# Kernel tuning notes

Hardware: AMD Instinct MI355X
Metric: run time of the kernel (lower is better)

## Reference

```python
import jax, jax.numpy as jnp
import numpy as np

B_GRAPHS = 32
EMB = 512
ESM = 1280
HEADS = 8
HEAD_DIM = EMB // HEADS


def _segments():
    lengths = 256 + 8 * np.arange(B_GRAPHS)          # 256..504, N = 12160
    batch_ids = np.repeat(np.arange(B_GRAPHS), lengths).astype(np.int32)
    pos = np.concatenate([np.arange(l) for l in lengths]).astype(np.int32)
    return batch_ids, pos, int(lengths.max()), int(lengths.sum())


def setup_inputs() -> dict:
    key = jax.random.key(0)
    ks = jax.random.split(key, 10)
    batch_ids, pos, pad_len, n = _segments()
    s = 0.02
    return {
        "esm_embedding": jax.random.normal(ks[0], (n, ESM), jnp.float32),
        "h": jax.random.normal(ks[1], (n, EMB), jnp.float32),
        "W_esm": jax.random.normal(ks[2], (EMB, ESM), jnp.float32) * s,
        "b_esm": jnp.zeros((EMB,), jnp.float32),
        "Wq": jax.random.normal(ks[3], (EMB, EMB), jnp.float32) * s,
        "bq": jnp.zeros((EMB,), jnp.float32),
        "Wk": jax.random.normal(ks[4], (EMB, EMB), jnp.float32) * s,
        "bk": jnp.zeros((EMB,), jnp.float32),
        "Wv": jax.random.normal(ks[5], (EMB, EMB), jnp.float32) * s,
        "bv": jnp.zeros((EMB,), jnp.float32),
        "Wo": jax.random.normal(ks[6], (EMB, EMB), jnp.float32) * s,
        "bo": jnp.zeros((EMB,), jnp.float32),
        "gamma": jnp.ones((EMB,), jnp.float32),
        "beta": jnp.zeros((EMB,), jnp.float32),
        "batch_ids": jnp.asarray(batch_ids),
        "pos": jnp.asarray(pos),
        "pad_len": pad_len,
        "num_graphs": B_GRAPHS,
    }


def _layer_norm(x, gamma, beta, eps=1e-5):
    mu = jnp.mean(x, axis=-1, keepdims=True)
    var = jnp.var(x, axis=-1, keepdims=True)
    return (x - mu) * jax.lax.rsqrt(var + eps) * gamma + beta


def reference(esm_embedding, h, W_esm, b_esm, Wq, bq, Wk, bk, Wv, bv, Wo, bo,
              gamma, beta, batch_ids, pos, pad_len, num_graphs):
    B, P, D, H, hd = num_graphs, pad_len, EMB, HEADS, HEAD_DIM
    residual = h
    # to_dense_batch: scatter nodes into [B, P, *] padded tensors + key mask
    h_dense = jnp.zeros((B, P, D), h.dtype).at[batch_ids, pos].set(h)
    h_mask = jnp.zeros((B, P), bool).at[batch_ids, pos].set(True)
    h_esm = esm_embedding @ W_esm.T + b_esm                      # [N, D]
    esm_dense = jnp.zeros((B, P, D), h.dtype).at[batch_ids, pos].set(h_esm)

    q = (h_dense @ Wq.T + bq).reshape(B, P, H, hd)
    k = (esm_dense @ Wk.T + bk).reshape(B, P, H, hd)
    v = (esm_dense @ Wv.T + bv).reshape(B, P, H, hd)

    scores = jnp.einsum("bqhd,bkhd->bhqk", q, k) / jnp.sqrt(jnp.float32(hd))
    scores = jnp.where(h_mask[:, None, None, :], scores, -jnp.inf)
    attn = jax.nn.softmax(scores, axis=-1)                        # [B,H,P,P]
    out = jnp.einsum("bhqk,bkhd->bqhd", attn, v).reshape(B, P, D)
    out = out @ Wo.T + bo
    out = out[batch_ids, pos]                                     # unpad -> [N, D]
    return _layer_norm(out + residual, gamma, beta)
```

## Files before the change

### kernel.cpp

```cpp
#include <hip/hip_runtime.h>

#define NTOT 12160
#define EMBD 512
#define ESMD 1280
#define NHEAD 8
#define HD 64
#define NG 32
#define NTILE 768

typedef __attribute__((ext_vector_type(8))) short short8v;
typedef __attribute__((ext_vector_type(4))) short short4v;
typedef __attribute__((ext_vector_type(4))) float floatx4;

__device__ inline short f2bf(float f) {
  union { float f; unsigned u; } v; v.f = f;
  unsigned r = v.u + 0x7fffu + ((v.u >> 16) & 1u);
  return (short)(r >> 16);
}

__device__ inline void gload_lds16(const void* g, void* l) {
  __builtin_amdgcn_global_load_lds((const __attribute__((address_space(1))) void*)g,
                                   (__attribute__((address_space(3))) void*)l, 16, 0, 0);
}

__device__ inline int node_graph(int n) {
  int g = (int)((sqrtf(3969.f + (float)n) - 63.f) * 0.5f);
  if (4 * (g + 1) * (g + 64) <= n) g++;
  else if (4 * g * (g + 63) > n) g--;
  return g;
}

__global__ __launch_bounds__(256) void cvt_kernel(
    const float* __restrict__ esm, const float* __restrict__ h,
    const float* __restrict__ Wq, const float* __restrict__ Wk,
    const float* __restrict__ Wv, const float* __restrict__ Wo,
    short* __restrict__ esm_b, short* __restrict__ h_b, short* __restrict__ Wq_b,
    short* __restrict__ Wk_b, short* __restrict__ Wv_b, short* __restrict__ Wo_b)
{
  int idx = blockIdx.x * 256 + threadIdx.x;
  const float* src; short* dst; int off;
  if      (idx < 3891200) { src = esm; dst = esm_b; off = idx; }
  else if (idx < 5447680) { src = h;   dst = h_b;   off = idx - 3891200; }
  else if (idx < 5513216) { src = Wq;  dst = Wq_b;  off = idx - 5447680; }
  else if (idx < 5578752) { src = Wk;  dst = Wk_b;  off = idx - 5513216; }
  else if (idx < 5644288) { src = Wv;  dst = Wv_b;  off = idx - 5578752; }
  else                    { src = Wo;  dst = Wo_b;  off = idx - 5644288; }
  const float4 v = *(const float4*)&src[(size_t)off * 4];
  short4v s; s[0] = f2bf(v.x); s[1] = f2bf(v.y); s[2] = f2bf(v.z); s[3] = f2bf(v.w);
  *(short4v*)&dst[(size_t)off * 4] = s;
}

__global__ __launch_bounds__(256) void wtrans_kernel(
    const float* __restrict__ W, short* __restrict__ WT)
{
  __shared__ short t[32][33];
  const int c0 = blockIdx.x * 32;
  const int r0 = blockIdx.y * 32;
  const int tr = threadIdx.x >> 5, tc = threadIdx.x & 31;
  for (int i = 0; i < 4; i++)
    t[i * 8 + tr][tc] = f2bf(W[(size_t)(r0 + i * 8 + tr) * 1280 + c0 + tc]);
  __syncthreads();
  for (int i = 0; i < 4; i++)
    WT[(size_t)(c0 + i * 8 + tr) * 512 + r0 + tc] = t[tc][i * 8 + tr];
}

__global__ __launch_bounds__(256) void bfuse_kernel(
    const float* __restrict__ Wk, const float* __restrict__ Wv,
    const float* __restrict__ besm, const float* __restrict__ bk,
    const float* __restrict__ bv, float* __restrict__ bkp, float* __restrict__ bvp)
{
  int wgid = blockIdx.x * 4 + (threadIdx.x >> 6);
  int lane = threadIdx.x & 63;
  const float* W  = (wgid < 512) ? Wk : Wv;
  const float* ba = (wgid < 512) ? bk : bv;
  float* o        = (wgid < 512) ? bkp : bvp;
  int row = wgid & 511;
  const float4 w0 = *(const float4*)&W[(size_t)row * 512 + lane * 8];
  const float4 w1 = *(const float4*)&W[(size_t)row * 512 + lane * 8 + 4];
  const float4 b0 = *(const float4*)&besm[lane * 8];
  const float4 b1 = *(const float4*)&besm[lane * 8 + 4];
  float s = w0.x * b0.x + w0.y * b0.y + w0.z * b0.z + w0.w * b0.w
          + w1.x * b1.x + w1.y * b1.y + w1.z * b1.z + w1.w * b1.w;
  for (int off = 1; off < 64; off <<= 1) s += __shfl_xor(s, off);
  if (lane == 0) o[row] = s + ba[row];
}

__device__ inline void gemm_core(const short* __restrict__ A, const short* __restrict__ W,
                                 int K, int row0, int col0,
                                 short* As, short* Bs, floatx4 acc[4][4])
{
  const int tid = threadIdx.x;
  const int lane = tid & 63, wave = tid >> 6;
  const int l15 = lane & 15, quad = lane >> 4;
  const int wm = (wave >> 1) * 64, wn = (wave & 1) * 64;
  const int lrow = lane >> 3;
  const int scol = ((lane & 7) ^ lrow) * 8;
  const int swz = l15 & 7;

  for (int k0 = 0; k0 < K; k0 += 64) {
    if (k0) __syncthreads();
    for (int p = 0; p < 4; p++) {
      int seg = wave * 4 + p;
      gload_lds16(&A[(size_t)(row0 + seg * 8 + lrow) * K + k0 + scol], &As[seg * 512]);
    }
    for (int p = 0; p < 4; p++) {
      int seg = wave * 4 + p;
      gload_lds16(&W[(size_t)(col0 + seg * 8 + lrow) * K + k0 + scol], &Bs[seg * 512]);
    }
    __syncthreads();
    for (int ks = 0; ks < 64; ks += 32) {
      const int off = (((ks >> 3) + quad) ^ swz) << 3;
      short8v a[4], b[4];
      for (int mt = 0; mt < 4; mt++)
        a[mt] = *(const short8v*)&As[(wm + mt * 16 + l15) * 64 + off];
      for (int nt = 0; nt < 4; nt++)
        b[nt] = *(const short8v*)&Bs[(wn + nt * 16 + l15) * 64 + off];
      for (int mt = 0; mt < 4; mt++)
        for (int nt = 0; nt < 4; nt++)
          acc[mt][nt] = __builtin_amdgcn_mfma_f32_16x16x32_bf16(a[mt], b[nt], acc[mt][nt], 0, 0, 0);
    }
  }
}

__device__ inline void epi_bf16(floatx4 acc[4][4], const float* bias, short* C,
                                int row0, int col0, int wm, int wn, int l15, int quad)
{
  for (int nt = 0; nt < 4; nt++) {
    int col = col0 + wn + nt * 16 + l15;
    float bv = bias[col];
    for (int mt = 0; mt < 4; mt++) {
      int rowb = row0 + wm + mt * 16 + quad * 4;
      for (int r = 0; r < 4; r++)
        C[(size_t)(rowb + r) * EMBD + col] = f2bf(acc[mt][nt][r] + bv);
    }
  }
}

__global__ __launch_bounds__(256) void wfuse_gemm(
    const short* __restrict__ Wk_b, const short* __restrict__ Wv_b,
    const short* __restrict__ WT, short* __restrict__ Wkp, short* __restrict__ Wvp)
{
  __shared__ short As[128 * 64];
  __shared__ short Bs[128 * 64];
  const int wh = blockIdx.x >= 10;
  const int col0 = (blockIdx.x - (wh ? 10 : 0)) * 128;
  const int row0 = blockIdx.y * 128;
  floatx4 acc[4][4];
  for (int i = 0; i < 4; i++) for (int j = 0; j < 4; j++)
    for (int r = 0; r < 4; r++) acc[i][j][r] = 0.f;
  gemm_core(wh ? Wv_b : Wk_b, WT, 512, row0, col0, As, Bs, acc);
  short* O = wh ? Wvp : Wkp;
  const int lane = threadIdx.x & 63, wave = threadIdx.x >> 6;
  const int l15 = lane & 15, quad = lane >> 4;
  const int wm = (wave >> 1) * 64, wn = (wave & 1) * 64;
  for (int nt = 0; nt < 4; nt++) {
    int col = col0 + wn + nt * 16 + l15;
    for (int mt = 0; mt < 4; mt++) {
      int rowb = row0 + wm + mt * 16 + quad * 4;
      for (int r = 0; r < 4; r++)
        O[(size_t)(rowb + r) * ESMD + col] = f2bf(acc[mt][nt][r]);
    }
  }
}

__global__ __launch_bounds__(512) void qkv_gemm(
    const short* __restrict__ hb, const short* __restrict__ esm_b,
    const short* __restrict__ Wq_b, const short* __restrict__ Wkp, const short* __restrict__ Wvp,
    const float* __restrict__ bq, const float* __restrict__ bkp, const float* __restrict__ bvp,
    short* __restrict__ qb, short* __restrict__ kp, short* __restrict__ vp)
{
  __shared__ short As[128 * 64];
  __shared__ short Bs[256 * 64];
  const int bid = blockIdx.x;
  const int xcd = bid & 7, idx = bid >> 3;
  const int rowc = idx / 6, c = idx - rowc * 6;
  const int r = xcd + 8 * rowc;
  if (r >= 95) return;
  const int row0 = r * 128;
  const int col0 = (c & 1) * 256;
  const int which = c >> 1;
  const short* A = (which == 0) ? hb : esm_b;
  const short* W = (which == 0) ? Wq_b : (which == 1 ? Wkp : Wvp);
  const int K = (which == 0) ? 512 : 1280;

  const int tid = threadIdx.x;
  const int lane = tid & 63, wave = tid >> 6;
  const int l15 = lane & 15, quad = lane >> 4;
  const int wm = (wave >> 2) * 64, wn = (wave & 3) * 64;
  const int lrow = lane >> 3;
  const int scol = ((lane & 7) ^ lrow) * 8;
  const int swz = l15 & 7;

  floatx4 acc[4][4];
  for (int i = 0; i < 4; i++) for (int j = 0; j < 4; j++)
    for (int rr = 0; rr < 4; rr++) acc[i][j][rr] = 0.f;

  for (int k0 = 0; k0 < K; k0 += 64) {
    if (k0) __syncthreads();
    for (int p = 0; p < 2; p++) {
      int seg = wave * 2 + p;
      gload_lds16(&A[(size_t)(row0 + seg * 8 + lrow) * K + k0 + scol], &As[seg * 512]);
    }
    for (int p = 0; p < 4; p++) {
      int seg = wave * 4 + p;
      gload_lds16(&W[(size_t)(col0 + seg * 8 + lrow) * K + k0 + scol], &Bs[seg * 512]);
    }
    __syncthreads();
    for (int ks = 0; ks < 64; ks += 32) {
      const int off = (((ks >> 3) + quad) ^ swz) << 3;
      short8v a[4], b[4];
      for (int mt = 0; mt < 4; mt++)
        a[mt] = *(const short8v*)&As[(wm + mt * 16 + l15) * 64 + off];
      for (int nt = 0; nt < 4; nt++)
        b[nt] = *(const short8v*)&Bs[(wn + nt * 16 + l15) * 64 + off];
      for (int mt = 0; mt < 4; mt++)
        for (int nt = 0; nt < 4; nt++)
          acc[mt][nt] = __builtin_amdgcn_mfma_f32_16x16x32_bf16(a[mt], b[nt], acc[mt][nt], 0, 0, 0);
    }
  }

  if (which == 0) {
    epi_bf16(acc, bq, qb, row0, col0, wm, wn, l15, quad);
  } else if (which == 1) {
    for (int mt = 0; mt < 4; mt++) {
      int rowb = row0 + wm + mt * 16 + quad * 4;
      int g = node_graph(rowb);
      int loc = rowb - 4 * g * (g + 63);
      int ptile = 16 * g + (g * g) / 4 + (loc >> 4);
      int l15k = loc & 15;
      for (int nt = 0; nt < 4; nt++) {
        int col = col0 + wn + nt * 16 + l15;
        float bv = bkp[col];
        int hh = col >> 6, dh = col & 63;
        int hfh = dh >> 5, qk = (dh & 31) >> 3, jk = dh & 7;
        size_t base = ((size_t)(hh * NTILE + ptile) * 2 + hfh) * 512
                      + (size_t)l15k * 32 + qk * 8 + jk;
        for (int rr = 0; rr < 4; rr++)
          kp[base + (size_t)rr * 32] = f2bf(acc[mt][nt][rr] + bv);
      }
    }
  } else {
    for (int mt = 0; mt < 4; mt++) {
      int rowb = row0 + wm + mt * 16 + quad * 4;
      int g = node_graph(rowb);
      int loc = rowb - 4 * g * (g + 63);
      int ptile = 16 * g + (g * g) / 4 + (loc >> 4);
      int koff = loc & 15;
      for (int nt = 0; nt < 4; nt++) {
        int col = col0 + wn + nt * 16 + l15;
        float bv = bvp[col];
        int hh = col >> 6, dh = col & 63;
        int dt = dh >> 4, l15v = dh & 15;
        size_t base = ((size_t)(hh * 4 + dt) * NTILE + ptile) * 256
                      + (size_t)l15v * 16 + koff;
        short4v sv;
        for (int rr = 0; rr < 4; rr++) sv[rr] = f2bf(acc[mt][nt][rr] + bv);
        *(short4v*)&vp[base] = sv;
      }
    }
  }
}

template<bool MASK>
__device__ inline void attn_chunk(
    int kc, int L, int Tg, int hb, int hdt4,
    const short* __restrict__ kp, const short* __restrict__ vp,
    short* Ps, const short8v& aq0, const short8v& aq1,
    floatx4 oacc[4], float rowsum[4], int l15, int quad)
{
  floatx4 s[4];
  const int t0 = Tg + (kc >> 4);
  for (int sub = 0; sub < 4; sub++) {
    const short* kpt = &kp[((size_t)(hb + t0 + sub) * 2) * 512 + l15 * 32 + quad * 8];
    short8v b0 = *(const short8v*)kpt;
    short8v b1 = *(const short8v*)(kpt + 512);
    floatx4 c; for (int r = 0; r < 4; r++) c[r] = 0.f;
    c = __builtin_amdgcn_mfma_f32_16x16x32_bf16(aq0, b0, c, 0, 0, 0);
    c = __builtin_amdgcn_mfma_f32_16x16x32_bf16(aq1, b1, c, 0, 0, 0);
    s[sub] = c;
  }
  for (int sub = 0; sub < 4; sub++)
    for (int r = 0; r < 4; r++) {
      float p = __expf(s[sub][r] * 0.125f);
      if (MASK && (kc + sub * 16 + l15 >= L)) p = 0.f;
      rowsum[r] += p;
      Ps[(quad * 4 + r) * 72 + sub * 16 + l15] = f2bf(p);
    }
  for (int half = 0; half < 2; half++) {
    short8v pA = *(const short8v*)&Ps[l15 * 72 + half * 32 + quad * 8];
    for (int dt = 0; dt < 4; dt++) {
      size_t vbase = ((size_t)(hdt4 + dt) * NTILE + t0 + half * 2 + (quad >> 1)) * 256
                     + (size_t)l15 * 16 + (quad & 1) * 8;
      short8v bvv = *(const short8v*)&vp[vbase];
      oacc[dt] = __builtin_amdgcn_mfma_f32_16x16x32_bf16(pA, bvv, oacc[dt], 0, 0, 0);
    }
  }
}

__global__ __launch_bounds__(512) void attn_kernel(
    const short* __restrict__ qb, const short* __restrict__ kp,
    const short* __restrict__ vp, short* __restrict__ ao)
{
  __shared__ short Ps_all[8][16 * 72];
  const int x = blockIdx.x & 7, j = blockIdx.x >> 3;
  int g = -1, qt = 0, accum = 0;
  for (int i = 0; i < 4; i++) {
    int gg = x + 8 * i;
    int t = 16 + ((gg + 1) >> 1);
    if (j < accum + t) { g = gg; qt = j - accum; break; }
    accum += t;
  }
  if (g < 0) return;
  const int L = 256 + 8 * g;
  const int start = 4 * g * (g + 63);
  const int Tg = 16 * g + (g * g) / 4;
  const int h = threadIdx.x >> 6;
  const int lane = threadIdx.x & 63;
  const int l15 = lane & 15, quad = lane >> 4;
  const int hb = h * NTILE, hdt4 = h * 4;
  short* Ps = Ps_all[h];

  int qrow = qt * 16 + l15;
  if (qrow > L - 1) qrow = L - 1;
  const size_t qoff = (size_t)(start + qrow) * EMBD + h * HD + quad * 8;
  const short8v aq0 = *(const short8v*)&qb[qoff];
  const short8v aq1 = *(const short8v*)&qb[qoff + 32];

  float rowsum[4];
  floatx4 oacc[4];
  for (int r = 0; r < 4; r++) rowsum[r] = 0.f;
  for (int dt = 0; dt < 4; dt++)
    for (int r = 0; r < 4; r++) oacc[dt][r] = 0.f;

  const int Lfull = L & ~63;
  for (int kc = 0; kc < Lfull; kc += 64)
    attn_chunk<false>(kc, L, Tg, hb, hdt4, kp, vp, Ps, aq0, aq1, oacc, rowsum, l15, quad);
  if (Lfull < L)
    attn_chunk<true>(Lfull, L, Tg, hb, hdt4, kp, vp, Ps, aq0, aq1, oacc, rowsum, l15, quad);

  float inv[4];
  for (int r = 0; r < 4; r++) {
    float red = rowsum[r];
    red += __shfl_xor(red, 1); red += __shfl_xor(red, 2);
    red += __shfl_xor(red, 4); red += __shfl_xor(red, 8);
    inv[r] = 1.f / red;
  }
  for (int dt = 0; dt < 4; dt++)
    for (int r = 0; r < 4; r++) {
      int rl = qt * 16 + quad * 4 + r;
      if (rl < L)
        ao[(size_t)(start + rl) * EMBD + h * HD + dt * 16 + l15] = f2bf(oacc[dt][r] * inv[r]);
    }
}

__global__ __launch_bounds__(256) void o_gemm(
    const short* __restrict__ A, const short* __restrict__ W,
    const float* __restrict__ bias, float* __restrict__ C)
{
  __shared__ short As[128 * 64];
  __shared__ short Bs[128 * 64];
  floatx4 acc[4][4];
  for (int i = 0; i < 4; i++) for (int j = 0; j < 4; j++)
    for (int r = 0; r < 4; r++) acc[i][j][r] = 0.f;
  const int row0 = blockIdx.y * 128, col0 = blockIdx.x * 128;
  gemm_core(A, W, EMBD, row0, col0, As, Bs, acc);
  const int lane = threadIdx.x & 63, wave = threadIdx.x >> 6;
  const int l15 = lane & 15, quad = lane >> 4;
  const int wm = (wave >> 1) * 64, wn = (wave & 1) * 64;
  for (int nt = 0; nt < 4; nt++) {
    int col = col0 + wn + nt * 16 + l15;
    float bv = bias[col];
    for (int mt = 0; mt < 4; mt++) {
      int rowb = row0 + wm + mt * 16 + quad * 4;
      for (int r = 0; r < 4; r++)
        C[(size_t)(rowb + r) * EMBD + col] = acc[mt][nt][r] + bv;
    }
  }
}

__global__ __launch_bounds__(64) void ln_kernel(
    float* __restrict__ y, const float* __restrict__ hres,
    const float* __restrict__ gamma, const float* __restrict__ beta)
{
  const int row = blockIdx.x;
  const int lane = threadIdx.x;
  const size_t base = (size_t)row * EMBD + lane * 8;
  const float4 a0 = *(const float4*)&y[base];
  const float4 a1 = *(const float4*)&y[base + 4];
  const float4 b0 = *(const float4*)&hres[base];
  const float4 b1 = *(const float4*)&hres[base + 4];
  float x[8] = { a0.x + b0.x, a0.y + b0.y, a0.z + b0.z, a0.w + b0.w,
                 a1.x + b1.x, a1.y + b1.y, a1.z + b1.z, a1.w + b1.w };
  float s = 0.f, s2 = 0.f;
  for (int i = 0; i < 8; i++) { s += x[i]; s2 += x[i] * x[i]; }
  for (int off = 1; off < 64; off <<= 1) { s += __shfl_xor(s, off); s2 += __shfl_xor(s2, off); }
  const float mu = s * (1.f / 512.f);
  const float var = s2 * (1.f / 512.f) - mu * mu;
  const float rstd = rsqrtf(var + 1e-5f);
  const float4 g0 = *(const float4*)&gamma[lane * 8];
  const float4 g1 = *(const float4*)&gamma[lane * 8 + 4];
  const float4 e0 = *(const float4*)&beta[lane * 8];
  const float4 e1 = *(const float4*)&beta[lane * 8 + 4];
  const float gg[8] = { g0.x, g0.y, g0.z, g0.w, g1.x, g1.y, g1.z, g1.w };
  const float ee[8] = { e0.x, e0.y, e0.z, e0.w, e1.x, e1.y, e1.z, e1.w };
  float o[8];
  for (int i = 0; i < 8; i++) o[i] = (x[i] - mu) * rstd * gg[i] + ee[i];
  *(float4*)&y[base]     = make_float4(o[0], o[1], o[2], o[3]);
  *(float4*)&y[base + 4] = make_float4(o[4], o[5], o[6], o[7]);
}

extern "C" void kernel_launch(void* const* d_in, const int* in_sizes, int n_in,
                              void* d_out, int out_size, void* d_ws, size_t ws_size,
                              hipStream_t stream)
{
  (void)in_sizes; (void)n_in; (void)out_size; (void)ws_size;
  const float* esm   = (const float*)d_in[0];
  const float* h     = (const float*)d_in[1];
  const float* Wesm  = (const float*)d_in[2];
  const float* besm  = (const float*)d_in[3];
  const float* Wq    = (const float*)d_in[4];
  const float* bq    = (const float*)d_in[5];
  const float* Wk    = (const float*)d_in[6];
  const float* bk    = (const float*)d_in[7];
  const float* Wv    = (const float*)d_in[8];
  const float* bv    = (const float*)d_in[9];
  const float* Wo    = (const float*)d_in[10];
  const float* bo    = (const float*)d_in[11];
  const float* gamma = (const float*)d_in[12];
  const float* beta  = (const float*)d_in[13];

  char* ws = (char*)d_ws;
  short* esm_b  = (short*)ws;
  short* ao     = esm_b;
  short* kp     = (short*)(ws + 31129600);
  short* WesmT  = kp;
  short* vp     = (short*)(ws + 43712512);
  short* Wq_b   = (short*)(ws + 56295424);
  short* Wk_b   = (short*)(ws + 56819712);
  short* Wv_b   = (short*)(ws + 57344000);
  short* Wo_b   = (short*)(ws + 57868288);
  short* Wkp    = (short*)(ws + 58392576);
  short* Wvp    = (short*)(ws + 59703296);
  float* bkp    = (float*)(ws + 61014016);
  float* bvp    = (float*)(ws + 61016064);
  short* qb     = (short*)d_out;
  short* h_b    = (short*)((char*)d_out + 12451840);
  float* y      = (float*)d_out;

  cvt_kernel<<<dim3(22304), dim3(256), 0, stream>>>(
      esm, h, Wq, Wk, Wv, Wo, esm_b, h_b, Wq_b, Wk_b, Wv_b, Wo_b);
  wtrans_kernel<<<dim3(40, 16), dim3(256), 0, stream>>>(Wesm, WesmT);
  bfuse_kernel<<<dim3(256), dim3(256), 0, stream>>>(Wk, Wv, besm, bk, bv, bkp, bvp);
  wfuse_gemm<<<dim3(20, 4), dim3(256), 0, stream>>>(Wk_b, Wv_b, WesmT, Wkp, Wvp);
  qkv_gemm<<<dim3(576), dim3(512), 0, stream>>>(
      h_b, esm_b, Wq_b, Wkp, Wvp, bq, bkp, bvp, qb, kp, vp);
  attn_kernel<<<dim3(832), dim3(512), 0, stream>>>(qb, kp, vp, ao);
  o_gemm<<<dim3(4, 95), dim3(256), 0, stream>>>(ao, Wo_b, bo, y);
  ln_kernel<<<dim3(NTOT), dim3(64), 0, stream>>>(y, h, gamma, beta);
}
```

Baseline: 309.0 us.

## Double-buffer GEMM LDS tiles, merge prep kernels, process two query tiles per wave

Merges the conversion, Wesm transpose and bias-fusion kernels into a single launch to cut launch overhead. Adds LDS double buffering to every GEMM core, so the next K-tile's global-to-LDS load is issued before computing on the current one. In attention, each wave now handles two 16-row query tiles, reusing each loaded K and V fragment twice and halving the grid. The cost is double LDS per GEMM block and more registers per attention wave, which may lower occupancy.

```diff
diff --git a/kernel.cpp b/kernel.cpp
--- a/kernel.cpp
+++ b/kernel.cpp
@@ -30,59 +30,55 @@
   return g;
 }
 
-__global__ __launch_bounds__(256) void cvt_kernel(
+__global__ __launch_bounds__(256) void prep_kernel(
     const float* __restrict__ esm, const float* __restrict__ h,
+    const float* __restrict__ Wesm, const float* __restrict__ besm,
     const float* __restrict__ Wq, const float* __restrict__ Wk,
     const float* __restrict__ Wv, const float* __restrict__ Wo,
+    const float* __restrict__ bk, const float* __restrict__ bv,
     short* __restrict__ esm_b, short* __restrict__ h_b, short* __restrict__ Wq_b,
-    short* __restrict__ Wk_b, short* __restrict__ Wv_b, short* __restrict__ Wo_b)
-{
-  int idx = blockIdx.x * 256 + threadIdx.x;
-  const float* src; short* dst; int off;
-  if      (idx < 3891200) { src = esm; dst = esm_b; off = idx; }
-  else if (idx < 5447680) { src = h;   dst = h_b;   off = idx - 3891200; }
-  else if (idx < 5513216) { src = Wq;  dst = Wq_b;  off = idx - 5447680; }
-  else if (idx < 5578752) { src = Wk;  dst = Wk_b;  off = idx - 5513216; }
-  else if (idx < 5644288) { src = Wv;  dst = Wv_b;  off = idx - 5578752; }
-  else                    { src = Wo;  dst = Wo_b;  off = idx - 5644288; }
-  const float4 v = *(const float4*)&src[(size_t)off * 4];
-  short4v s; s[0] = f2bf(v.x); s[1] = f2bf(v.y); s[2] = f2bf(v.z); s[3] = f2bf(v.w);
-  *(short4v*)&dst[(size_t)off * 4] = s;
-}
-
-__global__ __launch_bounds__(256) void wtrans_kernel(
-    const float* __restrict__ W, short* __restrict__ WT)
-{
-  __shared__ short t[32][33];
-  const int c0 = blockIdx.x * 32;
-  const int r0 = blockIdx.y * 32;
-  const int tr = threadIdx.x >> 5, tc = threadIdx.x & 31;
-  for (int i = 0; i < 4; i++)
-    t[i * 8 + tr][tc] = f2bf(W[(size_t)(r0 + i * 8 + tr) * 1280 + c0 + tc]);
-  __syncthreads();
-  for (int i = 0; i < 4; i++)
-    WT[(size_t)(c0 + i * 8 + tr) * 512 + r0 + tc] = t[tc][i * 8 + tr];
-}
-
-__global__ __launch_bounds__(256) void bfuse_kernel(
-    const float* __restrict__ Wk, const float* __restrict__ Wv,
-    const float* __restrict__ besm, const float* __restrict__ bk,
-    const float* __restrict__ bv, float* __restrict__ bkp, float* __restrict__ bvp)
-{
-  int wgid = blockIdx.x * 4 + (threadIdx.x >> 6);
-  int lane = threadIdx.x & 63;
-  const float* W  = (wgid < 512) ? Wk : Wv;
-  const float* ba = (wgid < 512) ? bk : bv;
-  float* o        = (wgid < 512) ? bkp : bvp;
-  int row = wgid & 511;
-  const float4 w0 = *(const float4*)&W[(size_t)row * 512 + lane * 8];
-  const float4 w1 = *(const float4*)&W[(size_t)row * 512 + lane * 8 + 4];
-  const float4 b0 = *(const float4*)&besm[lane * 8];
-  const float4 b1 = *(const float4*)&besm[lane * 8 + 4];
-  float s = w0.x * b0.x + w0.y * b0.y + w0.z * b0.z + w0.w * b0.w
-          + w1.x * b1.x + w1.y * b1.y + w1.z * b1.z + w1.w * b1.w;
-  for (int off = 1; off < 64; off <<= 1) s += __shfl_xor(s, off);
-  if (lane == 0) o[row] = s + ba[row];
+    short* __restrict__ Wk_b, short* __restrict__ Wv_b, short* __restrict__ Wo_b,
+    short* __restrict__ WT, float* __restrict__ bkp, float* __restrict__ bvp)
+{
+  const int b = blockIdx.x;
+  if (b < 22304) {
+    int idx = b * 256 + threadIdx.x;
+    const float* src; short* dst; int off;
+    if      (idx < 3891200) { src = esm; dst = esm_b; off = idx; }
+    else if (idx < 5447680) { src = h;   dst = h_b;   off = idx - 3891200; }
+    else if (idx < 5513216) { src = Wq;  dst = Wq_b;  off = idx - 5447680; }
+    else if (idx < 5578752) { src = Wk;  dst = Wk_b;  off = idx - 5513216; }
+    else if (idx < 5644288) { src = Wv;  dst = Wv_b;  off = idx - 5578752; }
+    else                    { src = Wo;  dst = Wo_b;  off = idx - 5644288; }
+    const float4 v = *(const float4*)&src[(size_t)off * 4];
+    short4v s; s[0] = f2bf(v.x); s[1] = f2bf(v.y); s[2] = f2bf(v.z); s[3] = f2bf(v.w);
+    *(short4v*)&dst[(size_t)off * 4] = s;
+  } else if (b < 22944) {
+    __shared__ short t[32][33];
+    const int bb = b - 22304;
+    const int c0 = (bb % 40) * 32, r0 = (bb / 40) * 32;
+    const int tr = threadIdx.x >> 5, tc = threadIdx.x & 31;
+    for (int i = 0; i < 4; i++)
+      t[i * 8 + tr][tc] = f2bf(Wesm[(size_t)(r0 + i * 8 + tr) * 1280 + c0 + tc]);
+    __syncthreads();
+    for (int i = 0; i < 4; i++)
+      WT[(size_t)(c0 + i * 8 + tr) * 512 + r0 + tc] = t[tc][i * 8 + tr];
+  } else {
+    int wgid = (b - 22944) * 4 + (threadIdx.x >> 6);
+    int lane = threadIdx.x & 63;
+    const float* W  = (wgid < 512) ? Wk : Wv;
+    const float* ba = (wgid < 512) ? bk : bv;
+    float* o        = (wgid < 512) ? bkp : bvp;
+    int row = wgid & 511;
+    const float4 w0 = *(const float4*)&W[(size_t)row * 512 + lane * 8];
+    const float4 w1 = *(const float4*)&W[(size_t)row * 512 + lane * 8 + 4];
+    const float4 b0 = *(const float4*)&besm[lane * 8];
+    const float4 b1 = *(const float4*)&besm[lane * 8 + 4];
+    float s = w0.x * b0.x + w0.y * b0.y + w0.z * b0.z + w0.w * b0.w
+            + w1.x * b1.x + w1.y * b1.y + w1.z * b1.z + w1.w * b1.w;
+    for (int off = 1; off < 64; off <<= 1) s += __shfl_xor(s, off);
+    if (lane == 0) o[row] = s + ba[row];
+  }
 }
 
 __device__ inline void gemm_core(const short* __restrict__ A, const short* __restrict__ W,
@@ -96,25 +92,32 @@
   const int lrow = lane >> 3;
   const int scol = ((lane & 7) ^ lrow) * 8;
   const int swz = l15 & 7;
-
-  for (int k0 = 0; k0 < K; k0 += 64) {
-    if (k0) __syncthreads();
-    for (int p = 0; p < 4; p++) {
-      int seg = wave * 4 + p;
-      gload_lds16(&A[(size_t)(row0 + seg * 8 + lrow) * K + k0 + scol], &As[seg * 512]);
-    }
-    for (int p = 0; p < 4; p++) {
-      int seg = wave * 4 + p;
-      gload_lds16(&W[(size_t)(col0 + seg * 8 + lrow) * K + k0 + scol], &Bs[seg * 512]);
-    }
+  const int niter = K >> 6;
+
+  for (int p = 0; p < 4; p++) {
+    int seg = wave * 4 + p;
+    gload_lds16(&A[(size_t)(row0 + seg * 8 + lrow) * K + scol], &As[seg * 512]);
+    gload_lds16(&W[(size_t)(col0 + seg * 8 + lrow) * K + scol], &Bs[seg * 512]);
+  }
+  for (int it = 0; it < niter; it++) {
+    const int cur = (it & 1) * 8192;
     __syncthreads();
+    if (it + 1 < niter) {
+      const int nxt = ((it + 1) & 1) * 8192;
+      const int k0 = (it + 1) << 6;
+      for (int p = 0; p < 4; p++) {
+        int seg = wave * 4 + p;
+        gload_lds16(&A[(size_t)(row0 + seg * 8 + lrow) * K + k0 + scol], &As[nxt + seg * 512]);
+        gload_lds16(&W[(size_t)(col0 + seg * 8 + lrow) * K + k0 + scol], &Bs[nxt + seg * 512]);
+      }
+    }
     for (int ks = 0; ks < 64; ks += 32) {
       const int off = (((ks >> 3) + quad) ^ swz) << 3;
       short8v a[4], b[4];
       for (int mt = 0; mt < 4; mt++)
-        a[mt] = *(const short8v*)&As[(wm + mt * 16 + l15) * 64 + off];
+        a[mt] = *(const short8v*)&As[cur + (wm + mt * 16 + l15) * 64 + off];
       for (int nt = 0; nt < 4; nt++)
-        b[nt] = *(const short8v*)&Bs[(wn + nt * 16 + l15) * 64 + off];
+        b[nt] = *(const short8v*)&Bs[cur + (wn + nt * 16 + l15) * 64 + off];
       for (int mt = 0; mt < 4; mt++)
         for (int nt = 0; nt < 4; nt++)
           acc[mt][nt] = __builtin_amdgcn_mfma_f32_16x16x32_bf16(a[mt], b[nt], acc[mt][nt], 0, 0, 0);
@@ -140,8 +143,8 @@
     const short* __restrict__ Wk_b, const short* __restrict__ Wv_b,
     const short* __restrict__ WT, short* __restrict__ Wkp, short* __restrict__ Wvp)
 {
-  __shared__ short As[128 * 64];
-  __shared__ short Bs[128 * 64];
+  __shared__ short As[2 * 128 * 64];
+  __shared__ short Bs[2 * 128 * 64];
   const int wh = blockIdx.x >= 10;
   const int col0 = (blockIdx.x - (wh ? 10 : 0)) * 128;
   const int row0 = blockIdx.y * 128;
@@ -169,8 +172,8 @@
     const float* __restrict__ bq, const float* __restrict__ bkp, const float* __restrict__ bvp,
     short* __restrict__ qb, short* __restrict__ kp, short* __restrict__ vp)
 {
-  __shared__ short As[128 * 64];
-  __shared__ short Bs[256 * 64];
+  __shared__ short As[2 * 128 * 64];
+  __shared__ short Bs[2 * 256 * 64];
   const int bid = blockIdx.x;
   const int xcd = bid & 7, idx = bid >> 3;
   const int rowc = idx / 6, c = idx - rowc * 6;
@@ -190,29 +193,42 @@
   const int lrow = lane >> 3;
   const int scol = ((lane & 7) ^ lrow) * 8;
   const int swz = l15 & 7;
+  const int niter = K >> 6;
 
   floatx4 acc[4][4];
   for (int i = 0; i < 4; i++) for (int j = 0; j < 4; j++)
     for (int rr = 0; rr < 4; rr++) acc[i][j][rr] = 0.f;
 
-  for (int k0 = 0; k0 < K; k0 += 64) {
-    if (k0) __syncthreads();
-    for (int p = 0; p < 2; p++) {
-      int seg = wave * 2 + p;
-      gload_lds16(&A[(size_t)(row0 + seg * 8 + lrow) * K + k0 + scol], &As[seg * 512]);
-    }
-    for (int p = 0; p < 4; p++) {
-      int seg = wave * 4 + p;
-      gload_lds16(&W[(size_t)(col0 + seg * 8 + lrow) * K + k0 + scol], &Bs[seg * 512]);
-    }
+  for (int p = 0; p < 2; p++) {
+    int seg = wave * 2 + p;
+    gload_lds16(&A[(size_t)(row0 + seg * 8 + lrow) * K + scol], &As[seg * 512]);
+  }
+  for (int p = 0; p < 4; p++) {
+    int seg = wave * 4 + p;
+    gload_lds16(&W[(size_t)(col0 + seg * 8 + lrow) * K + scol], &Bs[seg * 512]);
+  }
+  for (int it = 0; it < niter; it++) {
+    const int curA = (it & 1) * 8192, curB = (it & 1) * 16384;
     __syncthreads();
+    if (it + 1 < niter) {
+      const int nxtA = ((it + 1) & 1) * 8192, nxtB = ((it + 1) & 1) * 16384;
+      const int k0 = (it + 1) << 6;
+      for (int p = 0; p < 2; p++) {
+        int seg = wave * 2 + p;
+        gload_lds16(&A[(size_t)(row0 + seg * 8 + lrow) * K + k0 + scol], &As[nxtA + seg * 512]);
+      }
+      for (int p = 0; p < 4; p++) {
+        int seg = wave * 4 + p;
+        gload_lds16(&W[(size_t)(col0 + seg * 8 + lrow) * K + k0 + scol], &Bs[nxtB + seg * 512]);
+      }
+    }
     for (int ks = 0; ks < 64; ks += 32) {
       const int off = (((ks >> 3) + quad) ^ swz) << 3;
       short8v a[4], b[4];
       for (int mt = 0; mt < 4; mt++)
-        a[mt] = *(const short8v*)&As[(wm + mt * 16 + l15) * 64 + off];
+        a[mt] = *(const short8v*)&As[curA + (wm + mt * 16 + l15) * 64 + off];
       for (int nt = 0; nt < 4; nt++)
-        b[nt] = *(const short8v*)&Bs[(wn + nt * 16 + l15) * 64 + off];
+        b[nt] = *(const short8v*)&Bs[curB + (wn + nt * 16 + l15) * 64 + off];
       for (int mt = 0; mt < 4; mt++)
         for (int nt = 0; nt < 4; nt++)
           acc[mt][nt] = __builtin_amdgcn_mfma_f32_16x16x32_bf16(a[mt], b[nt], acc[mt][nt], 0, 0, 0);
@@ -262,37 +278,43 @@
 }
 
 template<bool MASK>
-__device__ inline void attn_chunk(
+__device__ inline void attn_chunk2(
     int kc, int L, int Tg, int hb, int hdt4,
     const short* __restrict__ kp, const short* __restrict__ vp,
-    short* Ps, const short8v& aq0, const short8v& aq1,
-    floatx4 oacc[4], float rowsum[4], int l15, int quad)
-{
-  floatx4 s[4];
+    short* Ps, const short8v aq0[2], const short8v aq1[2],
+    floatx4 oacc[2][4], float rowsum[2][4], int l15, int quad)
+{
+  floatx4 s[2][4];
   const int t0 = Tg + (kc >> 4);
   for (int sub = 0; sub < 4; sub++) {
     const short* kpt = &kp[((size_t)(hb + t0 + sub) * 2) * 512 + l15 * 32 + quad * 8];
     short8v b0 = *(const short8v*)kpt;
     short8v b1 = *(const short8v*)(kpt + 512);
-    floatx4 c; for (int r = 0; r < 4; r++) c[r] = 0.f;
-    c = __builtin_amdgcn_mfma_f32_16x16x32_bf16(aq0, b0, c, 0, 0, 0);
-    c = __builtin_amdgcn_mfma_f32_16x16x32_bf16(aq1, b1, c, 0, 0, 0);
-    s[sub] = c;
-  }
-  for (int sub = 0; sub < 4; sub++)
-    for (int r = 0; r < 4; r++) {
-      float p = __expf(s[sub][r] * 0.125f);
-      if (MASK && (kc + sub * 16 + l15 >= L)) p = 0.f;
-      rowsum[r] += p;
-      Ps[(quad * 4 + r) * 72 + sub * 16 + l15] = f2bf(p);
-    }
+    for (int q = 0; q < 2; q++) {
+      floatx4 cc; for (int r = 0; r < 4; r++) cc[r] = 0.f;
+      cc = __builtin_amdgcn_mfma_f32_16x16x32_bf16(aq0[q], b0, cc, 0, 0, 0);
+      cc = __builtin_amdgcn_mfma_f32_16x16x32_bf16(aq1[q], b1, cc, 0, 0, 0);
+      s[q][sub] = cc;
+    }
+  }
+  for (int q = 0; q < 2; q++)
+    for (int sub = 0; sub < 4; sub++)
+      for (int r = 0; r < 4; r++) {
+        float p = __expf(s[q][sub][r] * 0.125f);
+        if (MASK && (kc + sub * 16 + l15 >= L)) p = 0.f;
+        rowsum[q][r] += p;
+        Ps[q * 1152 + (quad * 4 + r) * 72 + sub * 16 + l15] = f2bf(p);
+      }
   for (int half = 0; half < 2; half++) {
-    short8v pA = *(const short8v*)&Ps[l15 * 72 + half * 32 + quad * 8];
+    short8v pA[2];
+    for (int q = 0; q < 2; q++)
+      pA[q] = *(const short8v*)&Ps[q * 1152 + l15 * 72 + half * 32 + quad * 8];
     for (int dt = 0; dt < 4; dt++) {
       size_t vbase = ((size_t)(hdt4 + dt) * NTILE + t0 + half * 2 + (quad >> 1)) * 256
                      + (size_t)l15 * 16 + (quad & 1) * 8;
       short8v bvv = *(const short8v*)&vp[vbase];
-      oacc[dt] = __builtin_amdgcn_mfma_f32_16x16x32_bf16(pA, bvv, oacc[dt], 0, 0, 0);
+      for (int q = 0; q < 2; q++)
+        oacc[q][dt] = __builtin_amdgcn_mfma_f32_16x16x32_bf16(pA[q], bvv, oacc[q][dt], 0, 0, 0);
     }
   }
 }
@@ -301,64 +323,74 @@
     const short* __restrict__ qb, const short* __restrict__ kp,
     const short* __restrict__ vp, short* __restrict__ ao)
 {
-  __shared__ short Ps_all[8][16 * 72];
+  __shared__ short Ps_all[8][2][16 * 72];
   const int x = blockIdx.x & 7, j = blockIdx.x >> 3;
-  int g = -1, qt = 0, accum = 0;
+  int g = -1, p2 = 0, accum = 0;
   for (int i = 0; i < 4; i++) {
     int gg = x + 8 * i;
-    int t = 16 + ((gg + 1) >> 1);
-    if (j < accum + t) { g = gg; qt = j - accum; break; }
-    accum += t;
+    int tq = 16 + ((gg + 1) >> 1);
+    int tp = (tq + 1) >> 1;
+    if (j < accum + tp) { g = gg; p2 = j - accum; break; }
+    accum += tp;
   }
   if (g < 0) return;
   const int L = 256 + 8 * g;
   const int start = 4 * g * (g + 63);
   const int Tg = 16 * g + (g * g) / 4;
+  const int T = 16 + ((g + 1) >> 1);
   const int h = threadIdx.x >> 6;
   const int lane = threadIdx.x & 63;
   const int l15 = lane & 15, quad = lane >> 4;
   const int hb = h * NTILE, hdt4 = h * 4;
-  short* Ps = Ps_all[h];
-
-  int qrow = qt * 16 + l15;
-  if (qrow > L - 1) qrow = L - 1;
-  const size_t qoff = (size_t)(start + qrow) * EMBD + h * HD + quad * 8;
-  const short8v aq0 = *(const short8v*)&qb[qoff];
-  const short8v aq1 = *(const short8v*)&qb[qoff + 32];
-
-  float rowsum[4];
-  floatx4 oacc[4];
-  for (int r = 0; r < 4; r++) rowsum[r] = 0.f;
-  for (int dt = 0; dt < 4; dt++)
-    for (int r = 0; r < 4; r++) oacc[dt][r] = 0.f;
+  short* Ps = &Ps_all[h][0][0];
+
+  int qt[2];
+  qt[0] = 2 * p2;
+  qt[1] = min(2 * p2 + 1, T - 1);
+  short8v aq0[2], aq1[2];
+  for (int q = 0; q < 2; q++) {
+    int qrow = qt[q] * 16 + l15;
+    if (qrow > L - 1) qrow = L - 1;
+    const size_t qoff = (size_t)(start + qrow) * EMBD + h * HD + quad * 8;
+    aq0[q] = *(const short8v*)&qb[qoff];
+    aq1[q] = *(const short8v*)&qb[qoff + 32];
+  }
+
+  float rowsum[2][4];
+  floatx4 oacc[2][4];
+  for (int q = 0; q < 2; q++)
+    for (int r = 0; r < 4; r++) { rowsum[q][r] = 0.f;
+      for (int dt = 0; dt < 4; dt++) oacc[q][dt][r] = 0.f; }
 
   const int Lfull = L & ~63;
   for (int kc = 0; kc < Lfull; kc += 64)
-    attn_chunk<false>(kc, L, Tg, hb, hdt4, kp, vp, Ps, aq0, aq1, oacc, rowsum, l15, quad);
+    attn_chunk2<false>(kc, L, Tg, hb, hdt4, kp, vp, Ps, aq0, aq1, oacc, rowsum, l15, quad);
   if (Lfull < L)
-    attn_chunk<true>(Lfull, L, Tg, hb, hdt4, kp, vp, Ps, aq0, aq1, oacc, rowsum, l15, quad);
-
-  float inv[4];
-  for (int r = 0; r < 4; r++) {
-    float red = rowsum[r];
-    red += __shfl_xor(red, 1); red += __shfl_xor(red, 2);
-    red += __shfl_xor(red, 4); red += __shfl_xor(red, 8);
-    inv[r] = 1.f / red;
-  }
-  for (int dt = 0; dt < 4; dt++)
+    attn_chunk2<true>(Lfull, L, Tg, hb, hdt4, kp, vp, Ps, aq0, aq1, oacc, rowsum, l15, quad);
+
+  for (int q = 0; q < 2; q++) {
+    float inv[4];
     for (int r = 0; r < 4; r++) {
-      int rl = qt * 16 + quad * 4 + r;
-      if (rl < L)
-        ao[(size_t)(start + rl) * EMBD + h * HD + dt * 16 + l15] = f2bf(oacc[dt][r] * inv[r]);
-    }
+      float red = rowsum[q][r];
+      red += __shfl_xor(red, 1); red += __shfl_xor(red, 2);
+      red += __shfl_xor(red, 4); red += __shfl_xor(red, 8);
+      inv[r] = 1.f / red;
+    }
+    for (int dt = 0; dt < 4; dt++)
+      for (int r = 0; r < 4; r++) {
+        int rl = qt[q] * 16 + quad * 4 + r;
+        if (rl < L)
+          ao[(size_t)(start + rl) * EMBD + h * HD + dt * 16 + l15] = f2bf(oacc[q][dt][r] * inv[r]);
+      }
+  }
 }
 
 __global__ __launch_bounds__(256) void o_gemm(
     const short* __restrict__ A, const short* __restrict__ W,
     const float* __restrict__ bias, float* __restrict__ C)
 {
-  __shared__ short As[128 * 64];
-  __shared__ short Bs[128 * 64];
+  __shared__ short As[2 * 128 * 64];
+  __shared__ short Bs[2 * 128 * 64];
   floatx4 acc[4][4];
   for (int i = 0; i < 4; i++) for (int j = 0; j < 4; j++)
     for (int r = 0; r < 4; r++) acc[i][j][r] = 0.f;
@@ -447,14 +479,13 @@
   short* h_b    = (short*)((char*)d_out + 12451840);
   float* y      = (float*)d_out;
 
-  cvt_kernel<<<dim3(22304), dim3(256), 0, stream>>>(
-      esm, h, Wq, Wk, Wv, Wo, esm_b, h_b, Wq_b, Wk_b, Wv_b, Wo_b);
-  wtrans_kernel<<<dim3(40, 16), dim3(256), 0, stream>>>(Wesm, WesmT);
-  bfuse_kernel<<<dim3(256), dim3(256), 0, stream>>>(Wk, Wv, besm, bk, bv, bkp, bvp);
+  prep_kernel<<<dim3(23200), dim3(256), 0, stream>>>(
+      esm, h, Wesm, besm, Wq, Wk, Wv, Wo, bk, bv,
+      esm_b, h_b, Wq_b, Wk_b, Wv_b, Wo_b, WesmT, bkp, bvp);
   wfuse_gemm<<<dim3(20, 4), dim3(256), 0, stream>>>(Wk_b, Wv_b, WesmT, Wkp, Wvp);
   qkv_gemm<<<dim3(576), dim3(512), 0, stream>>>(
       h_b, esm_b, Wq_b, Wkp, Wvp, bq, bkp, bvp, qb, kp, vp);
-  attn_kernel<<<dim3(832), dim3(512), 0, stream>>>(qb, kp, vp, ao);
+  attn_kernel<<<dim3(416), dim3(512), 0, stream>>>(qb, kp, vp, ao);
   o_gemm<<<dim3(4, 95), dim3(256), 0, stream>>>(ao, Wo_b, bo, y);
   ln_kernel<<<dim3(NTOT), dim3(64), 0, stream>>>(y, h, gamma, beta);
 }
```

Result: faster. 297.3 us (-3.8%).
